# Optimization experiments

Measured on AMD Instinct MI355X. Metric: run time of the kernel, lower is better.

## Reference

```python
import jax, jax.numpy as jnp
import numpy as np

B_, L_, D_MODEL = 2, 2048, 1024
D_INNER, D_STATE, DT_RANK, D_CONV = 2048, 16, 64, 4


def setup_inputs() -> dict:
    key = jax.random.key(0)
    ks = jax.random.split(key, 8)
    x = jax.random.normal(ks[0], (B_, L_, D_MODEL), dtype=jnp.float32)
    W_in = jax.random.normal(ks[1], (D_MODEL, 2 * D_INNER), dtype=jnp.float32) / np.sqrt(D_MODEL)
    conv_w = jax.random.normal(ks[2], (D_INNER, 1, D_CONV), dtype=jnp.float32) / np.sqrt(D_CONV)
    conv_b = jnp.zeros((D_INNER,), dtype=jnp.float32)
    W_x = jax.random.normal(ks[3], (D_INNER, DT_RANK + 2 * D_STATE), dtype=jnp.float32) / np.sqrt(D_INNER)
    W_dt = jax.random.normal(ks[4], (DT_RANK, D_INNER), dtype=jnp.float32) / np.sqrt(DT_RANK)
    b_dt = jax.random.normal(ks[5], (D_INNER,), dtype=jnp.float32) * 0.01
    A_log = jnp.log(jnp.broadcast_to(jnp.arange(1, D_STATE + 1, dtype=jnp.float32), (D_INNER, D_STATE)))
    D = jnp.ones((D_INNER,), dtype=jnp.float32)
    W_out = jax.random.normal(ks[6], (D_INNER, D_MODEL), dtype=jnp.float32) / np.sqrt(D_INNER)
    return {"x": x, "W_in": W_in, "conv_w": conv_w, "conv_b": conv_b, "W_x": W_x,
            "W_dt": W_dt, "b_dt": b_dt, "A_log": A_log, "D": D, "W_out": W_out}


def _mamba_fwd(x, W_in, conv_w, conv_b, W_x, W_dt, b_dt, A_log, D, W_out):
    b, l, d = x.shape
    x_and_res = x @ W_in                      # [b, l, 2*d_inner]
    xi, res = jnp.split(x_and_res, 2, axis=-1)
    # causal depthwise conv1d (torch pads d_conv-1 both sides then truncates -> left pad only)
    xc = jax.lax.conv_general_dilated(
        xi.transpose(0, 2, 1), conv_w, window_strides=(1,),
        padding=[(D_CONV - 1, 0)], feature_group_count=D_INNER,
        dimension_numbers=("NCH", "OIH", "NCH"))
    xc = (xc + conv_b[None, :, None]).transpose(0, 2, 1)  # [b, l, d_inner]
    xc = jax.nn.silu(xc)
    # SSM params
    x_dbl = xc @ W_x                           # [b, l, dt_rank + 2n]
    delta, Bm, Cm = jnp.split(x_dbl, [DT_RANK, DT_RANK + D_STATE], axis=-1)
    delta = jax.nn.softplus(delta @ W_dt + b_dt)          # [b, l, d_inner]
    A = -jnp.exp(A_log.astype(jnp.float32))               # [d_inner, n]
    deltaA = jnp.exp(jnp.einsum('bld,dn->bldn', delta, A))
    deltaB_u = jnp.einsum('bld,bln,bld->bldn', delta, Bm, xc)
    # sequential selective scan over l via lax.scan
    def step(h, inp):
        dA, dBu, c = inp           # [b,d,n], [b,d,n], [b,n]
        h = dA * h + dBu
        y = jnp.einsum('bdn,bn->bd', h, c)
        return h, y
    h0 = jnp.zeros((b, D_INNER, D_STATE), dtype=jnp.float32)
    _, ys = jax.lax.scan(step, h0, (deltaA.transpose(1, 0, 2, 3),
                                    deltaB_u.transpose(1, 0, 2, 3),
                                    Cm.transpose(1, 0, 2)))
    y = ys.transpose(1, 0, 2)                 # [b, l, d_inner]
    y = y + xc * D
    y = y * jax.nn.silu(res)
    return y @ W_out


def reference(x, W_in, conv_w, conv_b, W_x, W_dt, b_dt, A_log, D, W_out):
    return _mamba_fwd(x, W_in, conv_w, conv_b, W_x, W_dt, b_dt, A_log, D, W_out)
```

## Files before the change

### kernel.cpp

```cpp
#include <hip/hip_runtime.h>
#include <hip/hip_bf16.h>
#include <cstdint>


#define B_    2
#define L_    2048
#define DMODEL 1024
#define DINNER 2048
#define DSTATE 16
#define DTRANK 64
#define NC    16
#define CL    128

typedef short bf16x8 __attribute__((ext_vector_type(8)));
typedef float f32x4  __attribute__((ext_vector_type(4)));

__device__ __forceinline__ float sigmoidf_(float x) {
  return 1.f / (1.f + __expf(-x));
}
__device__ __forceinline__ float softplusf_(float x) {
  return fmaxf(x, 0.f) + log1pf(__expf(-fabsf(x)));
}
__device__ __forceinline__ unsigned short f2bf_rne(float x) {
  union { float f; unsigned int u; } v; v.f = x;
  unsigned int r = v.u + 0x7FFFu + ((v.u >> 16) & 1u);
  return (unsigned short)(r >> 16);
}
__device__ __forceinline__ float bf2f(unsigned short h) {
  union { float f; unsigned int u; } v; v.u = ((unsigned int)h) << 16;
  return v.f;
}
__device__ __forceinline__ void split3_a(float x, unsigned short* o) {
  unsigned short hi = f2bf_rne(x);
  unsigned short lo = f2bf_rne(x - bf2f(hi));
  o[0] = hi; o[1] = lo; o[2] = hi;
}
__device__ __forceinline__ void split3_b(float x, unsigned short* o) {
  unsigned short hi = f2bf_rne(x);
  unsigned short lo = f2bf_rne(x - bf2f(hi));
  o[0] = hi; o[1] = hi; o[2] = lo;
}

__device__ __forceinline__ void gload16(const void* g, void* l) {
  __builtin_amdgcn_global_load_lds(
      (const __attribute__((address_space(1))) void*)g,
      (__attribute__((address_space(3))) void*)l, 16, 0, 0);
}

template<int SPLITCOL>
__launch_bounds__(256)
__global__ void gemm_mfma_bf16(const unsigned short* __restrict__ A3,
                               const unsigned short* __restrict__ B3t,
                               float* __restrict__ outA,
                               float* __restrict__ outB,
                               int N, int K3)
{
  __shared__ unsigned short As[128 * 64];
  __shared__ unsigned short Bs[128 * 64];

  const int tid  = threadIdx.x;
  const int lane = tid & 63;
  const int wid  = tid >> 6;
  const int wr   = wid >> 1;
  const int wc   = wid & 1;
  const int m0   = blockIdx.y * 128;
  const int n0   = blockIdx.x * 128;

  const int srow = lane >> 3;
  const int scol = ((lane & 7) ^ srow) * 8;

  const unsigned short* gA = A3 + (size_t)(m0 + wid * 8 + srow) * K3 + scol;
  const unsigned short* gB = B3t + (size_t)(n0 + wid * 8 + srow) * K3 + scol;
  const size_t rs32 = (size_t)32 * K3;

  unsigned short* lA = &As[wid * 8 * 64];
  unsigned short* lB = &Bs[wid * 8 * 64];

  f32x4 acc[4][4];
#pragma unroll
  for (int i = 0; i < 4; ++i)
#pragma unroll
    for (int j = 0; j < 4; ++j) acc[i][j] = (f32x4){0.f, 0.f, 0.f, 0.f};

  const int KT = K3 >> 6;
  for (int kt = 0; kt < KT; ++kt) {
    const int k0 = kt << 6;
#pragma unroll
    for (int i = 0; i < 4; ++i) {
      gload16(gA + i * rs32 + k0, lA + i * 32 * 64);
      gload16(gB + i * rs32 + k0, lB + i * 32 * 64);
    }
    __syncthreads();

#pragma unroll
    for (int kk = 0; kk < 2; ++kk) {
      const int c16 = kk * 4 + (lane >> 4);
      bf16x8 a[4], b[4];
#pragma unroll
      for (int rb = 0; rb < 4; ++rb) {
        const int row = wr * 64 + rb * 16 + (lane & 15);
        a[rb] = *(const bf16x8*)&As[row * 64 + ((c16 ^ (row & 7)) << 3)];
        const int col = wc * 64 + rb * 16 + (lane & 15);
        b[rb] = *(const bf16x8*)&Bs[col * 64 + ((c16 ^ (col & 7)) << 3)];
      }
#pragma unroll
      for (int rb = 0; rb < 4; ++rb)
#pragma unroll
        for (int nb = 0; nb < 4; ++nb)
          acc[rb][nb] = __builtin_amdgcn_mfma_f32_16x16x32_bf16(
              a[rb], b[nb], acc[rb][nb], 0, 0, 0);
    }
    __syncthreads();
  }

  const int crow0 = (lane >> 4) * 4;
  const int ccol  = lane & 15;
#pragma unroll
  for (int rb = 0; rb < 4; ++rb) {
#pragma unroll
    for (int nb = 0; nb < 4; ++nb) {
      const int gc = n0 + wc * 64 + nb * 16 + ccol;
#pragma unroll
      for (int j = 0; j < 4; ++j) {
        const int gr = m0 + wr * 64 + rb * 16 + crow0 + j;
        const float v = acc[rb][nb][j];
        if (SPLITCOL > 0) {
          if (gc < SPLITCOL) outA[(size_t)gr * SPLITCOL + gc] = v;
          else               outB[(size_t)gr * SPLITCOL + (gc - SPLITCOL)] = v;
        } else {
          outA[(size_t)gr * N + gc] = v;
        }
      }
    }
  }
}

__launch_bounds__(256)
__global__ void split_a3(const float* __restrict__ in,
                         unsigned short* __restrict__ out)
{
  const int idx = blockIdx.x * 256 + threadIdx.x;
  const int row = idx >> 8;
  const int q   = idx & 255;
  float4 v = *(const float4*)&in[(size_t)row * DMODEL + q * 4];
  unsigned short buf[12] __attribute__((aligned(8)));
  split3_a(v.x, &buf[0]);
  split3_a(v.y, &buf[3]);
  split3_a(v.z, &buf[6]);
  split3_a(v.w, &buf[9]);
  unsigned short* o = out + (size_t)row * 3072 + q * 12;
#pragma unroll
  for (int j = 0; j < 3; ++j)
    *(ushort4*)&o[j * 4] = *(const ushort4*)&buf[j * 4];
}

__launch_bounds__(256)
__global__ void split_bt3(const float* __restrict__ B,
                          unsigned short* __restrict__ out,
                          int K, int N)
{
  __shared__ float T[64][65];
  const int n0 = blockIdx.x * 64;
  const int k0 = blockIdx.y * 64;
  const int t  = threadIdx.x;

  const int nl4 = (t & 15) * 4;
  const int klr = t >> 4;
#pragma unroll
  for (int i = 0; i < 4; ++i) {
    float4 v = *(const float4*)&B[(size_t)(k0 + klr + i * 16) * N + n0 + nl4];
    T[klr + i * 16][nl4 + 0] = v.x;
    T[klr + i * 16][nl4 + 1] = v.y;
    T[klr + i * 16][nl4 + 2] = v.z;
    T[klr + i * 16][nl4 + 3] = v.w;
  }
  __syncthreads();

  const int nl = t >> 2;
  const int kc = (t & 3) * 16;
  unsigned short buf[48] __attribute__((aligned(8)));
#pragma unroll
  for (int kk = 0; kk < 16; ++kk) split3_b(T[kc + kk][nl], &buf[kk * 3]);
  unsigned short* o = out + (size_t)(n0 + nl) * (3 * K) + 3 * (k0 + kc);
#pragma unroll
  for (int j = 0; j < 12; ++j)
    *(ushort4*)&o[j * 4] = *(const ushort4*)&buf[j * 4];
}

template<int BM, int BN, int BK, int RG, int CG, int EPI>
__launch_bounds__(256)
__global__ void gemm_f32(const float* __restrict__ A, int lda,
                         const float* __restrict__ B, int ldb,
                         float* __restrict__ C, int ldc,
                         int M, int N, int K,
                         const float* __restrict__ bias)
{
  __shared__ float As[BK][BM + 4];
  __shared__ float Bs[BK][BN + 4];

  const int tid = threadIdx.x;
  const int tx = tid & 15;
  const int ty = tid >> 4;
  const int m0 = blockIdx.y * BM;
  const int n0 = blockIdx.x * BN;

  float acc[RG * 4][CG * 4];
#pragma unroll
  for (int i = 0; i < RG * 4; ++i)
#pragma unroll
    for (int j = 0; j < CG * 4; ++j) acc[i][j] = 0.f;

  const int KF4 = BK / 4;
  const int NF4 = BN / 4;

  for (int k0 = 0; k0 < K; k0 += BK) {
#pragma unroll
    for (int j = tid; j < BM * KF4; j += 256) {
      int row = j / KF4, kq = j % KF4;
      float4 v = *(const float4*)&A[(size_t)(m0 + row) * lda + k0 + kq * 4];
      As[kq * 4 + 0][row] = v.x;
      As[kq * 4 + 1][row] = v.y;
      As[kq * 4 + 2][row] = v.z;
      As[kq * 4 + 3][row] = v.w;
    }
#pragma unroll
    for (int j = tid; j < BK * NF4; j += 256) {
      int row = j / NF4, nq = j % NF4;
      int c = n0 + nq * 4;
      float4 v;
      if (c + 3 < N) {
        v = *(const float4*)&B[(size_t)(k0 + row) * ldb + c];
      } else {
        const float* bp = &B[(size_t)(k0 + row) * ldb];
        v.x = (c + 0 < N) ? bp[c + 0] : 0.f;
        v.y = (c + 1 < N) ? bp[c + 1] : 0.f;
        v.z = (c + 2 < N) ? bp[c + 2] : 0.f;
        v.w = (c + 3 < N) ? bp[c + 3] : 0.f;
      }
      *(float4*)&Bs[row][nq * 4] = v;
    }
    __syncthreads();

#pragma unroll
    for (int k = 0; k < BK; ++k) {
      float a[RG][4], b[CG][4];
#pragma unroll
      for (int g = 0; g < RG; ++g) {
        float4 va = *(const float4*)&As[k][g * (BM / RG) + ty * 4];
        a[g][0] = va.x; a[g][1] = va.y; a[g][2] = va.z; a[g][3] = va.w;
      }
#pragma unroll
      for (int h = 0; h < CG; ++h) {
        float4 vb = *(const float4*)&Bs[k][h * (BN / CG) + tx * 4];
        b[h][0] = vb.x; b[h][1] = vb.y; b[h][2] = vb.z; b[h][3] = vb.w;
      }
#pragma unroll
      for (int g = 0; g < RG; ++g)
#pragma unroll
        for (int i = 0; i < 4; ++i)
#pragma unroll
          for (int h = 0; h < CG; ++h)
#pragma unroll
            for (int j = 0; j < 4; ++j)
              acc[g * 4 + i][h * 4 + j] =
                  fmaf(a[g][i], b[h][j], acc[g * 4 + i][h * 4 + j]);
    }
    __syncthreads();
  }

#pragma unroll
  for (int g = 0; g < RG; ++g) {
#pragma unroll
    for (int i = 0; i < 4; ++i) {
      int r = m0 + g * (BM / RG) + ty * 4 + i;
#pragma unroll
      for (int h = 0; h < CG; ++h) {
        int c = n0 + h * (BN / CG) + tx * 4;
        float4 v;
        v.x = acc[g * 4 + i][h * 4 + 0];
        v.y = acc[g * 4 + i][h * 4 + 1];
        v.z = acc[g * 4 + i][h * 4 + 2];
        v.w = acc[g * 4 + i][h * 4 + 3];
        if (c + 3 < N) {
          if (EPI == 1) {
            v.x = softplusf_(v.x + bias[c + 0]);
            v.y = softplusf_(v.y + bias[c + 1]);
            v.z = softplusf_(v.z + bias[c + 2]);
            v.w = softplusf_(v.w + bias[c + 3]);
          }
          *(float4*)&C[(size_t)r * ldc + c] = v;
        } else {
          float vv[4] = {v.x, v.y, v.z, v.w};
#pragma unroll
          for (int j = 0; j < 4; ++j)
            if (c + j < N) {
              float o = vv[j];
              if (EPI == 1) o = softplusf_(o + bias[c + j]);
              C[(size_t)r * ldc + c + j] = o;
            }
        }
      }
    }
  }
}

__launch_bounds__(256)
__global__ void conv_silu(const float* __restrict__ xi,
                          const float* __restrict__ conv_w,
                          const float* __restrict__ conv_b,
                          float* __restrict__ xc)
{
  const int total = B_ * L_ * (DINNER / 4);
  for (int idx = blockIdx.x * blockDim.x + threadIdx.x; idx < total;
       idx += gridDim.x * blockDim.x) {
    int d4 = idx & (DINNER / 4 - 1);
    int l = (idx >> 9) & (L_ - 1);
    int b = idx >> 20;
    int d = d4 * 4;

    float w[4][4];
#pragma unroll
    for (int c = 0; c < 4; ++c) {
      float4 wv = *(const float4*)&conv_w[(d + c) * 4];
      w[c][0] = wv.x; w[c][1] = wv.y; w[c][2] = wv.z; w[c][3] = wv.w;
    }
    float4 bv = *(const float4*)&conv_b[d];
    float s[4] = {bv.x, bv.y, bv.z, bv.w};
#pragma unroll
    for (int t = 0; t < 4; ++t) {
      int ls = l - 3 + t;
      if (ls >= 0) {
        float4 xv = *(const float4*)&xi[(size_t)(b * L_ + ls) * DINNER + d];
        s[0] = fmaf(w[0][t], xv.x, s[0]);
        s[1] = fmaf(w[1][t], xv.y, s[1]);
        s[2] = fmaf(w[2][t], xv.z, s[2]);
        s[3] = fmaf(w[3][t], xv.w, s[3]);
      }
    }
    float4 o;
    o.x = s[0] * sigmoidf_(s[0]);
    o.y = s[1] * sigmoidf_(s[1]);
    o.z = s[2] * sigmoidf_(s[2]);
    o.w = s[3] * sigmoidf_(s[3]);
    *(float4*)&xc[(size_t)idx * 4] = o;
  }
}

__launch_bounds__(256)
__global__ void scan_pass1(const float* __restrict__ delta,
                           const float* __restrict__ xc,
                           const float* __restrict__ xdbl,
                           const float* __restrict__ A_log,
                           float* __restrict__ Pbuf,
                           float* __restrict__ Qbuf)
{
  const int blk = blockIdx.x;
  const int b = blk >> 7;
  const int c = (blk >> 3) & (NC - 1);
  const int d = ((blk & 7) << 8) + threadIdx.x;

  float An[DSTATE];
#pragma unroll
  for (int n = 0; n < DSTATE; ++n) An[n] = -__expf(A_log[d * DSTATE + n]);

  __shared__ float bs[CL][DSTATE];
  const size_t bL = (size_t)b * L_;
  const int l0 = c * CL;
  for (int j = threadIdx.x; j < CL * 4; j += 256) {
    int step = j >> 2, q = j & 3;
    *(float4*)&bs[step][q * 4] =
        *(const float4*)&xdbl[(bL + l0 + step) * 96 + DTRANK + q * 4];
  }
  __syncthreads();

  float P[DSTATE], q[DSTATE];
#pragma unroll
  for (int n = 0; n < DSTATE; ++n) { P[n] = 1.f; q[n] = 0.f; }

  for (int i = 0; i < CL; ++i) {
    const size_t bl = bL + l0 + i;
    float dv = delta[bl * DINNER + d];
    float dx = dv * xc[bl * DINNER + d];
#pragma unroll
    for (int n = 0; n < DSTATE; ++n) {
      float dA = __expf(dv * An[n]);
      P[n] *= dA;
      q[n] = fmaf(dA, q[n], dx * bs[i][n]);
    }
  }
  const size_t base = (((size_t)b * NC + c) * DSTATE) * DINNER + d;
#pragma unroll
  for (int n = 0; n < DSTATE; ++n) {
    Pbuf[base + (size_t)n * DINNER] = P[n];
    Qbuf[base + (size_t)n * DINNER] = q[n];
  }
}

__launch_bounds__(256)
__global__ void scan_combine(const float* __restrict__ Pbuf,
                             const float* __restrict__ Qbuf,
                             float* __restrict__ Hini)
{
  const int idx = blockIdx.x * 256 + threadIdx.x;
  const int d = idx & (DINNER - 1);
  const int n = (idx >> 11) & (DSTATE - 1);
  const int b = idx >> 15;

  float h = 0.f;
#pragma unroll
  for (int c = 0; c < NC; ++c) {
    const size_t off = (((size_t)b * NC + c) * DSTATE + n) * DINNER + d;
    Hini[off] = h;
    h = fmaf(Pbuf[off], h, Qbuf[off]);
  }
}

__launch_bounds__(256)
__global__ void scan_pass2(const float* __restrict__ delta,
                           const float* __restrict__ xc,
                           const float* __restrict__ res,
                           const float* __restrict__ xdbl,
                           const float* __restrict__ A_log,
                           const float* __restrict__ Dvec,
                           const float* __restrict__ Hini,
                           unsigned short* __restrict__ yg3)
{
  const int blk = blockIdx.x;
  const int b = blk >> 7;
  const int c = (blk >> 3) & (NC - 1);
  const int d = ((blk & 7) << 8) + threadIdx.x;

  float An[DSTATE];
#pragma unroll
  for (int n = 0; n < DSTATE; ++n) An[n] = -__expf(A_log[d * DSTATE + n]);
  const float Dd = Dvec[d];

  float h[DSTATE];
  const size_t base = (((size_t)b * NC + c) * DSTATE) * DINNER + d;
#pragma unroll
  for (int n = 0; n < DSTATE; ++n) h[n] = Hini[base + (size_t)n * DINNER];

  __shared__ float bc[CL][2 * DSTATE];
  const size_t bL = (size_t)b * L_;
  const int l0 = c * CL;
  for (int j = threadIdx.x; j < CL * 8; j += 256) {
    int step = j >> 3, q = j & 7;
    *(float4*)&bc[step][q * 4] =
        *(const float4*)&xdbl[(bL + l0 + step) * 96 + DTRANK + q * 4];
  }
  __syncthreads();

  for (int i = 0; i < CL; ++i) {
    const size_t bl = bL + l0 + i;
    float dv = delta[bl * DINNER + d];
    float xv = xc[bl * DINNER + d];
    float rv = res[bl * DINNER + d];
    float dx = dv * xv;
    float y = 0.f;
#pragma unroll
    for (int n = 0; n < DSTATE; ++n) {
      float dA = __expf(dv * An[n]);
      h[n] = fmaf(dA, h[n], dx * bc[i][n]);
      y = fmaf(h[n], bc[i][DSTATE + n], y);
    }
    float v = (y + xv * Dd) * (rv * sigmoidf_(rv));
    unsigned short hi = f2bf_rne(v);
    unsigned short lo = f2bf_rne(v - bf2f(hi));
    const size_t o = bl * 6144 + 3 * (size_t)d;
    yg3[o + 0] = hi; yg3[o + 1] = lo; yg3[o + 2] = hi;
  }
}

extern "C" void kernel_launch(void* const* d_in, const int* in_sizes, int n_in,
                              void* d_out, int out_size, void* d_ws,
                              size_t ws_size, hipStream_t stream)
{
  const float* x      = (const float*)d_in[0];
  const float* W_in   = (const float*)d_in[1];
  const float* conv_w = (const float*)d_in[2];
  const float* conv_b = (const float*)d_in[3];
  const float* W_x    = (const float*)d_in[4];
  const float* W_dt   = (const float*)d_in[5];
  const float* b_dt   = (const float*)d_in[6];
  const float* A_log  = (const float*)d_in[7];
  const float* Dv     = (const float*)d_in[8];
  const float* W_out  = (const float*)d_in[9];
  float* out = (float*)d_out;

  float* ws = (float*)d_ws;
  float* xi    = ws;
  float* res   = ws + 8388608;
  float* xc    = ws + 16777216;
  float* xdbl  = ws + 25165824;
  float* Pbuf  = ws + 25559040;
  float* Qbuf  = ws + 26607616;
  float* Hini  = ws + 27656192;
  unsigned short* yg3      = (unsigned short*)(ws + 28704768);
  unsigned short* bt3_wout = (unsigned short*)(ws + 41287680);
  unsigned short* a3_x     = (unsigned short*)(ws + 16777216);
  unsigned short* bt3_win  = (unsigned short*)(ws + 23068672);
  float* delta = ws;

  const int M = B_ * L_;

  split_a3<<<4096, 256, 0, stream>>>(x, a3_x);
  split_bt3<<<dim3(4096 / 64, 1024 / 64), 256, 0, stream>>>(W_in, bt3_win,
                                                            1024, 4096);

  gemm_mfma_bf16<2048><<<dim3(32, 32), 256, 0, stream>>>(
      a3_x, bt3_win, xi, res, 4096, 3072);

  split_bt3<<<dim3(1024 / 64, 2048 / 64), 256, 0, stream>>>(W_out, bt3_wout,
                                                            2048, 1024);

  conv_silu<<<4096, 256, 0, stream>>>(xi, conv_w, conv_b, xc);

  gemm_f32<64, 64, 16, 1, 1, 0><<<dim3(2, M / 64), 256, 0, stream>>>(
      xc, DINNER, W_x, 96, xdbl, 96, M, 96, DINNER, nullptr);

  gemm_f32<128, 128, 16, 2, 2, 1>
      <<<dim3(DINNER / 128, M / 128), 256, 0, stream>>>(
          xdbl, 96, W_dt, DINNER, delta, DINNER, M, DINNER, DTRANK, b_dt);

  scan_pass1<<<B_ * NC * (DINNER / 256), 256, 0, stream>>>(
      delta, xc, xdbl, A_log, Pbuf, Qbuf);
  scan_combine<<<(B_ * DSTATE * DINNER) / 256, 256, 0, stream>>>(
      Pbuf, Qbuf, Hini);
  scan_pass2<<<B_ * NC * (DINNER / 256), 256, 0, stream>>>(
      delta, xc, res, xdbl, A_log, Dv, Hini, yg3);

  gemm_mfma_bf16<0><<<dim3(8, 32), 256, 0, stream>>>(
      yg3, bt3_wout, out, nullptr, 1024, 6144);
}
```

Before: 759.1 us.

## Replace x_proj GEMM with split-K kernel plus reduction pass

The small-N (96) x_proj GEMM previously ran on a 2x64 grid of 64x64 tiles, giving only 128 blocks. It now splits K=2048 into 4 chunks over a 4x256 grid of 384-thread blocks, each thread computing four outputs from direct global float4 loads. A separate reduce kernel then sums the four partials into xdbl. This is meant to raise parallelism and occupancy, at the cost of an extra launch, a partial buffer written into the workspace (reusing the xi region), and no shared-memory reuse of W_x.

```diff
diff --git a/kernel.cpp b/kernel.cpp
--- a/kernel.cpp
+++ b/kernel.cpp
@@ -185,6 +185,62 @@
 #pragma unroll
   for (int j = 0; j < 12; ++j)
     *(ushort4*)&o[j * 4] = *(const ushort4*)&buf[j * 4];
+}
+
+#define KS_   4
+#define KCH   (DINNER / KS_)
+__launch_bounds__(384)
+__global__ void gemm_wx_splitk(const float* __restrict__ xc,
+                               const float* __restrict__ wx,
+                               float* __restrict__ part)
+{
+  const int ks = blockIdx.x;
+  const int m0 = blockIdx.y * 16;
+  const int t  = threadIdx.x;
+  const int r  = t / 24;
+  const int c  = (t % 24) * 4;
+  const int k0 = ks * KCH;
+
+  const float* arow = xc + (size_t)(m0 + r) * DINNER + k0;
+  const float* wp   = wx + (size_t)k0 * 96 + c;
+
+  float ax = 0.f, ay = 0.f, az = 0.f, aw = 0.f;
+  for (int k = 0; k < KCH; k += 4) {
+    float4 a  = *(const float4*)&arow[k];
+    float4 w0 = *(const float4*)&wp[(size_t)(k + 0) * 96];
+    float4 w1 = *(const float4*)&wp[(size_t)(k + 1) * 96];
+    float4 w2 = *(const float4*)&wp[(size_t)(k + 2) * 96];
+    float4 w3 = *(const float4*)&wp[(size_t)(k + 3) * 96];
+    ax = fmaf(a.x, w0.x, ax); ax = fmaf(a.y, w1.x, ax);
+    ax = fmaf(a.z, w2.x, ax); ax = fmaf(a.w, w3.x, ax);
+    ay = fmaf(a.x, w0.y, ay); ay = fmaf(a.y, w1.y, ay);
+    ay = fmaf(a.z, w2.y, ay); ay = fmaf(a.w, w3.y, ay);
+    az = fmaf(a.x, w0.z, az); az = fmaf(a.y, w1.z, az);
+    az = fmaf(a.z, w2.z, az); az = fmaf(a.w, w3.z, az);
+    aw = fmaf(a.x, w0.w, aw); aw = fmaf(a.y, w1.w, aw);
+    aw = fmaf(a.z, w2.w, aw); aw = fmaf(a.w, w3.w, aw);
+  }
+  float4 o = {ax, ay, az, aw};
+  *(float4*)&part[((size_t)ks * 4096 + m0 + r) * 96 + c] = o;
+}
+
+__launch_bounds__(256)
+__global__ void reduce_wx(const float* __restrict__ part,
+                          float* __restrict__ xdbl)
+{
+  const int i = blockIdx.x * 256 + threadIdx.x;
+  const size_t S = (size_t)4096 * 96 / 4;
+  const float4* p = (const float4*)part;
+  float4 a = p[i];
+  float4 b = p[i + S];
+  float4 c = p[i + 2 * S];
+  float4 d = p[i + 3 * S];
+  float4 o;
+  o.x = (a.x + b.x) + (c.x + d.x);
+  o.y = (a.y + b.y) + (c.y + d.y);
+  o.z = (a.z + b.z) + (c.z + d.z);
+  o.w = (a.w + b.w) + (c.w + d.w);
+  ((float4*)xdbl)[i] = o;
 }
 
 template<int BM, int BN, int BK, int RG, int CG, int EPI>
@@ -500,6 +556,7 @@
   unsigned short* a3_x     = (unsigned short*)(ws + 16777216);
   unsigned short* bt3_win  = (unsigned short*)(ws + 23068672);
   float* delta = ws;
+  float* part  = ws;
 
   const int M = B_ * L_;
 
@@ -515,8 +572,8 @@
 
   conv_silu<<<4096, 256, 0, stream>>>(xi, conv_w, conv_b, xc);
 
-  gemm_f32<64, 64, 16, 1, 1, 0><<<dim3(2, M / 64), 256, 0, stream>>>(
-      xc, DINNER, W_x, 96, xdbl, 96, M, 96, DINNER, nullptr);
+  gemm_wx_splitk<<<dim3(KS_, M / 16), 384, 0, stream>>>(xc, W_x, part);
+  reduce_wx<<<384, 256, 0, stream>>>(part, xdbl);
 
   gemm_f32<128, 128, 16, 2, 2, 1>
       <<<dim3(DINNER / 128, M / 128), 256, 0, stream>>>(
```

New measurement: 703.5 us. 1.08x faster.
